# Kernel optimization log

Hardware: AMD Instinct MI355X
Metric: run time of the kernel (lower is better)

Reference implementation:

```python
import jax, jax.numpy as jnp
import numpy as np
from jax import lax

B, S, E, CC, H, NH, K = 8, 2048, 128, 256, 256, 8, 7
HD = H // NH  # head dim = 32


def setup_inputs() -> dict:
    key = jax.random.key(0)
    ks = jax.random.split(key, 16)
    x = jax.random.normal(ks[0], (B, S, E), dtype=jnp.float32)
    lengths = jax.random.randint(ks[1], (B,), S // 2, S + 1)
    mask = (jnp.arange(S)[None, :] < lengths[:, None])  # contiguous prefix padding mask
    sc = 0.02
    return {
        "x": x,
        "mask": mask,
        "conv_w": jax.random.normal(ks[2], (CC, E, K), dtype=jnp.float32) * sc,
        "conv_b": jnp.zeros((CC,), jnp.float32),
        "wq": jax.random.normal(ks[3], (CC, H), dtype=jnp.float32) * sc,
        "bq": jnp.zeros((H,), jnp.float32),
        "wk": jax.random.normal(ks[4], (CC, H), dtype=jnp.float32) * sc,
        "bk": jnp.zeros((H,), jnp.float32),
        "wv": jax.random.normal(ks[5], (CC, H), dtype=jnp.float32) * sc,
        "bv": jnp.zeros((H,), jnp.float32),
        "fc_w": jax.random.normal(ks[6], (H, CC), dtype=jnp.float32) * sc,
        "fc_b": jnp.zeros((CC,), jnp.float32),
        "ln_g": jnp.ones((CC,), jnp.float32),
        "ln_b": jnp.zeros((CC,), jnp.float32),
        "gamma": jnp.float32(0.5),
        "std_param": jnp.float32(0.2),
    }


def _penalty(mask, gamma, std_param):
    # (B, S, S) Gaussian penalty, nonzero only in the valid_len x valid_len block
    valid_len = mask.sum(axis=-1).astype(jnp.float32)  # (B,)
    idx = jnp.arange(S, dtype=jnp.float32)
    valid = (jnp.arange(S)[None, :] < mask.sum(axis=-1)[:, None]).astype(jnp.float32)  # (B,S)
    norm_pos = (idx[None, :] + 1.0) / (valid_len[:, None] + 1.0)  # (B,S)
    std = jnp.clip(std_param, 0.01, 0.5)
    base = jnp.exp(-((norm_pos - 0.5) ** 2) / (2.0 * std * std))
    pvec = base * (jnp.exp(gamma) - 1.0) * valid  # (B,S)
    pen = 0.5 * (pvec[:, :, None] + pvec[:, None, :])
    return pen * valid[:, :, None] * valid[:, None, :]


def reference(x, mask, conv_w, conv_b, wq, bq, wk, bk, wv, bv, fc_w, fc_b, ln_g, ln_b, gamma, std_param):
    # Conv1d frontend: (B,S,E) -> (B,E,S) -> conv -> relu -> (B,S,CC)
    xt = jnp.transpose(x, (0, 2, 1))
    y = lax.conv_general_dilated(xt, conv_w, window_strides=(1,), padding=[(K // 2, K // 2)])
    y = jax.nn.relu(y + conv_b[None, :, None])
    h = jnp.transpose(y, (0, 2, 1))  # (B,S,CC)

    q = (h @ wq + bq).reshape(B, S, NH, HD).transpose(0, 2, 1, 3)
    k = (h @ wk + bk).reshape(B, S, NH, HD).transpose(0, 2, 1, 3)
    v = (h @ wv + bv).reshape(B, S, NH, HD).transpose(0, 2, 1, 3)

    scores = jnp.einsum('bnqd,bnkd->bnqk', q, k) / np.sqrt(HD).astype(np.float32)
    scores = scores - _penalty(mask, gamma, std_param)[:, None, :, :]
    scores = jnp.where(mask[:, None, None, :], scores, jnp.float32(-1e10))
    probs = jax.nn.softmax(scores, axis=-1)
    ctx = jnp.einsum('bnqk,bnkd->bnqd', probs, v)
    ctx = ctx.transpose(0, 2, 1, 3).reshape(B, S, H)
    out = ctx @ fc_w + fc_b

    z = h + out
    mu = z.mean(-1, keepdims=True)
    var = ((z - mu) ** 2).mean(-1, keepdims=True)
    return (z - mu) / jnp.sqrt(var + 1e-5) * ln_g + ln_b
```

## Files before the change

kernel.cpp:

```cpp
#include <hip/hip_runtime.h>
#include <hip/hip_bf16.h>

#define B_ 8
#define S_ 2048
#define E_ 128
#define CC_ 256
#define H_ 256
#define NH_ 8
#define HD_ 32
#define KW_ 7

typedef __attribute__((ext_vector_type(8))) short bf16x8;
typedef __attribute__((ext_vector_type(4))) float f32x4;
typedef __attribute__((ext_vector_type(16))) float f32x16;

#define QSCALE_ (0.17677669529663687f * 1.4426950408889634f)
#define CPEN_   0.7213475204444817f

static __device__ __forceinline__ unsigned short f2bf(float f) {
    __hip_bfloat16 h = __float2bfloat16(f);
    return *(unsigned short*)&h;
}
static __device__ __forceinline__ float bf2f(unsigned short u) {
    __hip_bfloat16 h = *(__hip_bfloat16*)&u;
    return __bfloat162float(h);
}
static __device__ __forceinline__ void perm32swap(unsigned& a, unsigned& b) {
    asm volatile("s_nop 1\n\tv_permlane32_swap_b32 %0, %1" : "+v"(a), "+v"(b));
}

__global__ __launch_bounds__(256) void reorder_convw(
    const float* __restrict__ cw, unsigned short* __restrict__ wre2)
{
    int i = blockIdx.x * 256 + threadIdx.x;
    int kl = i & 31, cc = (i >> 5) & 255, eb = (i >> 13) & 3, kk = i >> 15;
    wre2[i] = f2bf(cw[cc * (E_ * KW_) + (eb * 32 + kl) * KW_ + kk]);
}
__global__ __launch_bounds__(256) void reorder_qkvw(
    const float* __restrict__ wq, const float* __restrict__ wk,
    const float* __restrict__ wv, unsigned short* __restrict__ wqkv2)
{
    int i = blockIdx.x * 256 + threadIdx.x;
    int kl = i & 31, col = (i >> 5) & 255, kb = (i >> 13) & 7, m = i >> 16;
    const float* W = (m == 0) ? wq : (m == 1) ? wk : wv;
    wqkv2[i] = f2bf(W[(kb * 32 + kl) * H_ + col]);
}
__global__ __launch_bounds__(256) void reorder_fcw(
    const float* __restrict__ fw, unsigned short* __restrict__ wf2)
{
    int i = blockIdx.x * 256 + threadIdx.x;
    int kl = i & 31, col = (i >> 5) & 255, kb = i >> 13;
    wf2[i] = f2bf(fw[(kb * 32 + kl) * CC_ + col]);
}

__global__ __launch_bounds__(256) void penalty_kernel(
    const void* __restrict__ mask, const float* __restrict__ gamma_p,
    const float* __restrict__ std_p, float* __restrict__ pvec,
    int* __restrict__ lenv)
{
    __shared__ int cnt[256];
    int b = blockIdx.x, tid = threadIdx.x;

    uint32_t w0 = ((const uint32_t*)mask)[0];
    int mode = 0;
    if (w0 == 0x01010101u) mode = 1;
    else if (w0 == 0x3F803F80u) mode = 2;
    else if (w0 == 0x3F800000u) mode = 3;

    int c = 0;
    for (int s = tid; s < S_; s += 256) {
        bool vv;
        size_t i = (size_t)b * S_ + s;
        if (mode == 0)      vv = ((const int*)mask)[i] != 0;
        else if (mode == 1) vv = ((const unsigned char*)mask)[i] != 0;
        else if (mode == 2) vv = (((const unsigned short*)mask)[i] & 0x7FFFu) != 0;
        else                vv = ((const float*)mask)[i] != 0.f;
        c += vv ? 1 : 0;
    }
    cnt[tid] = c;
    __syncthreads();
    for (int off = 128; off > 0; off >>= 1) {
        if (tid < off) cnt[tid] += cnt[tid + off];
        __syncthreads();
    }
    int L = cnt[0];
    if (tid == 0) lenv[b] = L;

    float Lf = (float)L;
    float gamma = gamma_p[0];
    float sd = std_p[0];
    sd = fminf(fmaxf(sd, 0.01f), 0.5f);
    float scale = expf(gamma) - 1.f;
    float inv2s2 = 1.f / (2.f * sd * sd);
    for (int s = tid; s < S_; s += 256) {
        float np = (s + 1.f) / (Lf + 1.f);
        float e = np - 0.5f;
        float base = expf(-(e * e) * inv2s2);
        pvec[(size_t)b * S_ + s] = (s < L) ? base * scale : 0.f;
    }
}

__global__ __launch_bounds__(256) void conv_mfma_kernel(
    const float* __restrict__ x, const unsigned short* __restrict__ wre2,
    const float* __restrict__ cb, unsigned short* __restrict__ hb)
{
    __shared__ short xl[70][136];
    const int tid = threadIdx.x, wave = tid >> 6, lane = tid & 63;
    const int l15 = lane & 15, l4 = lane >> 4;
    const int s0 = blockIdx.x * 64, b = blockIdx.y;

    for (int idx = tid; idx < 70 * 32; idx += 256) {
        int row = idx >> 5, c4 = idx & 31;
        int pos = s0 - 3 + row;
        float4 v = {0.f, 0.f, 0.f, 0.f};
        if (pos >= 0 && pos < S_)
            v = *(const float4*)(x + ((size_t)b * S_ + pos) * E_ + c4 * 4);
        short* p = &xl[row][c4 * 4];
        p[0] = (short)f2bf(v.x); p[1] = (short)f2bf(v.y);
        p[2] = (short)f2bf(v.z); p[3] = (short)f2bf(v.w);
    }
    __syncthreads();

    f32x4 acc[4][4];
#pragma unroll
    for (int i = 0; i < 4; i++)
#pragma unroll
        for (int j = 0; j < 4; j++) acc[i][j] = (f32x4){0.f, 0.f, 0.f, 0.f};

#pragma unroll 1
    for (int kk = 0; kk < KW_; kk++) {
#pragma unroll
        for (int eb = 0; eb < 4; eb++) {
            const unsigned short* wp =
                wre2 + (((size_t)(kk * 4 + eb) * 256 + wave * 64 + l15) * 32) + l4 * 8;
            bf16x8 af[4], bfr[4];
#pragma unroll
            for (int ct = 0; ct < 4; ct++)
                bfr[ct] = *(const bf16x8*)(wp + ct * 512);
#pragma unroll
            for (int rt = 0; rt < 4; rt++)
                af[rt] = *(const bf16x8*)(&xl[rt * 16 + l15 + kk][eb * 32 + l4 * 8]);
#pragma unroll
            for (int rt = 0; rt < 4; rt++)
#pragma unroll
                for (int ct = 0; ct < 4; ct++)
                    acc[rt][ct] = __builtin_amdgcn_mfma_f32_16x16x32_bf16(
                        af[rt], bfr[ct], acc[rt][ct], 0, 0, 0);
        }
    }

#pragma unroll
    for (int ct = 0; ct < 4; ct++) {
        int col = wave * 64 + ct * 16 + l15;
        float bias = cb[col];
#pragma unroll
        for (int rt = 0; rt < 4; rt++)
#pragma unroll
            for (int r = 0; r < 4; r++) {
                float v0 = acc[rt][ct][r] + bias;
                v0 = v0 > 0.f ? v0 : 0.f;
                int row = s0 + rt * 16 + l4 * 4 + r;
                hb[((size_t)b * S_ + row) * CC_ + col] = f2bf(v0);
            }
    }
}

__global__ __launch_bounds__(256) void qkv_mfma_kernel(
    const unsigned short* __restrict__ hb, const unsigned short* __restrict__ wqkv2,
    const float* __restrict__ bq, const float* __restrict__ bk,
    const float* __restrict__ bv,
    unsigned short* __restrict__ qo, unsigned short* __restrict__ ko,
    unsigned short* __restrict__ vo)
{
    __shared__ short Al[64][264];
    const int tid = threadIdx.x, wave = tid >> 6, lane = tid & 63;
    const int l15 = lane & 15, l4 = lane >> 4;
    const int s0 = blockIdx.x * 64, b = blockIdx.y;

    for (int idx = tid; idx < 64 * 32; idx += 256) {
        int row = idx >> 5, c8 = idx & 31;
        *(bf16x8*)(&Al[row][c8 * 8]) =
            *(const bf16x8*)(hb + ((size_t)b * S_ + s0 + row) * CC_ + c8 * 8);
    }
    __syncthreads();

#pragma unroll 1
    for (int m = 0; m < 3; m++) {
        f32x4 acc[4][4];
#pragma unroll
        for (int i = 0; i < 4; i++)
#pragma unroll
            for (int j = 0; j < 4; j++) acc[i][j] = (f32x4){0.f, 0.f, 0.f, 0.f};

#pragma unroll 1
        for (int kb8 = 0; kb8 < 8; kb8++) {
            const unsigned short* wp =
                wqkv2 + (((size_t)(m * 8 + kb8) * 256 + wave * 64 + l15) * 32) + l4 * 8;
            bf16x8 af[4], bfr[4];
#pragma unroll
            for (int ct = 0; ct < 4; ct++)
                bfr[ct] = *(const bf16x8*)(wp + ct * 512);
#pragma unroll
            for (int rt = 0; rt < 4; rt++)
                af[rt] = *(const bf16x8*)(&Al[rt * 16 + l15][kb8 * 32 + l4 * 8]);
#pragma unroll
            for (int rt = 0; rt < 4; rt++)
#pragma unroll
                for (int ct = 0; ct < 4; ct++)
                    acc[rt][ct] = __builtin_amdgcn_mfma_f32_16x16x32_bf16(
                        af[rt], bfr[ct], acc[rt][ct], 0, 0, 0);
        }

        const float* bias_p = (m == 0) ? bq : (m == 1) ? bk : bv;
        unsigned short* O = (m == 0) ? qo : (m == 1) ? ko : vo;
        const float oscale = (m == 0) ? QSCALE_ : 1.f;
#pragma unroll
        for (int ct = 0; ct < 4; ct++) {
            int col = wave * 64 + ct * 16 + l15;
            float bias = bias_p[col];
            int n = col >> 5, d = col & 31;
#pragma unroll
            for (int rt = 0; rt < 4; rt++)
#pragma unroll
                for (int r = 0; r < 4; r++) {
                    int row = s0 + rt * 16 + l4 * 4 + r;
                    O[(((size_t)b * NH_ + n) * S_ + row) * HD_ + d] =
                        f2bf((acc[rt][ct][r] + bias) * oscale);
                }
        }
    }
}

__global__ __launch_bounds__(256) void attn_mfma_kernel(
    const unsigned short* __restrict__ q, const unsigned short* __restrict__ k,
    const unsigned short* __restrict__ v, const float* __restrict__ pvec,
    const int* __restrict__ lenv, unsigned short* __restrict__ ctxb)
{
    __shared__ short Kt[2][128][40];
    __shared__ short Vt[2][32][136];
    __shared__ __align__(16) float ctC[2][2][128];

    const int tid = threadIdx.x;
    const int wave = tid >> 6, lane = tid & 63;
    const int r31 = lane & 31, hi = lane >> 5;
    const int hi8 = hi * 8, hi4 = hi * 4;
    const int n = blockIdx.y, b = blockIdx.z;
    const int qrow = blockIdx.x * 128 + wave * 32 + r31;
    const int L = lenv[b];
    const int nt = (L + 127) >> 7;

    const size_t head = ((size_t)b * NH_ + n) * S_;
    const unsigned short* qbase = q + head * HD_;
    const unsigned short* kbase = k + head * HD_;
    const unsigned short* vbase = v + head * HD_;

    bf16x8 qf0 = *(const bf16x8*)(qbase + (size_t)qrow * HD_ + hi8);
    bf16x8 qf1 = *(const bf16x8*)(qbase + (size_t)qrow * HD_ + 16 + hi8);
    const int crow = (qrow < L) ? 1 : 0;

    f32x16 acc;
#pragma unroll
    for (int r = 0; r < 16; r++) acc[r] = 0.f;
    float m_r = -1e30f, l_r = 0.f;

    const int krow = tid >> 1, kch = (tid & 1) * 16;
    const int d7x2 = 2 * (r31 & 7);
    const int vc = krow >> 3, vk7 = krow & 7;

    bf16x8 kreg0, kreg1, va, vb;
    float pvr = 0.f;

    kreg0 = *(const bf16x8*)(kbase + (size_t)krow * HD_ + kch);
    kreg1 = *(const bf16x8*)(kbase + (size_t)krow * HD_ + kch + 8);
    va    = *(const bf16x8*)(vbase + (size_t)krow * HD_ + kch);
    vb    = *(const bf16x8*)(vbase + (size_t)krow * HD_ + kch + 8);
    if (tid < 128) pvr = pvec[(size_t)b * S_ + tid];
    {
        *(bf16x8*)(&Kt[0][krow][kch])     = kreg0;
        *(bf16x8*)(&Kt[0][krow][kch + 8]) = kreg1;
#pragma unroll
        for (int i = 0; i < 8; i++) {
            int d0 = kch + i, d1 = kch + 8 + i;
            Vt[0][d0][((((vc - 2 * (d0 & 7)) & 7) | (vc & 8)) << 3) + vk7] = va[i];
            Vt[0][d1][((((vc - 2 * (d1 & 7)) & 7) | (vc & 8)) << 3) + vk7] = vb[i];
        }
        if (tid < 128) {
            bool vkk = tid < L;
            ctC[0][0][tid] = vkk ? 0.f : -1e10f;
            ctC[0][1][tid] = vkk ? (-CPEN_ * pvr) : -1e10f;
        }
    }
    __syncthreads();

#pragma unroll 1
    for (int t = 0; t < nt; t++) {
        const int cur = t & 1;
        const int knext = (t + 1) << 7;
        const bool more = (t + 1 < nt);

        if (more) {
            kreg0 = *(const bf16x8*)(kbase + (size_t)(knext + krow) * HD_ + kch);
            kreg1 = *(const bf16x8*)(kbase + (size_t)(knext + krow) * HD_ + kch + 8);
            va    = *(const bf16x8*)(vbase + (size_t)(knext + krow) * HD_ + kch);
            vb    = *(const bf16x8*)(vbase + (size_t)(knext + krow) * HD_ + kch + 8);
            if (tid < 128) pvr = pvec[(size_t)b * S_ + knext + tid];
        }

        __builtin_amdgcn_s_setprio(1);
        f32x16 sc[4];
#pragma unroll
        for (int t4 = 0; t4 < 4; t4++) {
            bf16x8 kf0 = *(const bf16x8*)(&Kt[cur][t4 * 32 + r31][hi8]);
            bf16x8 kf1 = *(const bf16x8*)(&Kt[cur][t4 * 32 + r31][16 + hi8]);
            f32x16 c0;
#pragma unroll
            for (int g = 0; g < 4; g++) {
                f32x4 cp = *(const f32x4*)(&ctC[cur][crow][t4 * 32 + g * 8 + hi4]);
#pragma unroll
                for (int j = 0; j < 4; j++) c0[g * 4 + j] = cp[j];
            }
            f32x16 s1 = __builtin_amdgcn_mfma_f32_32x32x16_bf16(kf0, qf0, c0, 0, 0, 0);
            sc[t4] = __builtin_amdgcn_mfma_f32_32x32x16_bf16(kf1, qf1, s1, 0, 0, 0);
        }
        __builtin_amdgcn_s_setprio(0);

        float pmx = -1e30f;
#pragma unroll
        for (int t4 = 0; t4 < 4; t4++)
#pragma unroll
            for (int r = 0; r < 16; r += 2)
                pmx = fmaxf(pmx, fmaxf(sc[t4][r], sc[t4][r + 1]));
        pmx = fmaxf(pmx, __shfl_xor(pmx, 32, 64));

        float alpha = 1.f;
        if (!__all(pmx <= m_r + 8.f)) {
            float mn = fmaxf(m_r, pmx);
            alpha = exp2f(m_r - mn);
            m_r = mn;
#pragma unroll
            for (int r = 0; r < 16; r++) acc[r] *= alpha;
        }

        float rs = 0.f;
        unsigned pk[4][8];
#pragma unroll
        for (int t4 = 0; t4 < 4; t4++) {
            float p[16];
#pragma unroll
            for (int r = 0; r < 16; r++) {
                p[r] = exp2f(sc[t4][r] - m_r);
                rs += p[r];
            }
            unsigned U00 = (unsigned)f2bf(p[0])  | ((unsigned)f2bf(p[1])  << 16);
            unsigned U01 = (unsigned)f2bf(p[2])  | ((unsigned)f2bf(p[3])  << 16);
            unsigned U10 = (unsigned)f2bf(p[4])  | ((unsigned)f2bf(p[5])  << 16);
            unsigned U11 = (unsigned)f2bf(p[6])  | ((unsigned)f2bf(p[7])  << 16);
            unsigned U20 = (unsigned)f2bf(p[8])  | ((unsigned)f2bf(p[9])  << 16);
            unsigned U21 = (unsigned)f2bf(p[10]) | ((unsigned)f2bf(p[11]) << 16);
            unsigned U30 = (unsigned)f2bf(p[12]) | ((unsigned)f2bf(p[13]) << 16);
            unsigned U31 = (unsigned)f2bf(p[14]) | ((unsigned)f2bf(p[15]) << 16);
            perm32swap(U00, U10);
            perm32swap(U01, U11);
            perm32swap(U20, U30);
            perm32swap(U21, U31);
            pk[t4][0] = U00; pk[t4][1] = U01; pk[t4][2] = U10; pk[t4][3] = U11;
            pk[t4][4] = U20; pk[t4][5] = U21; pk[t4][6] = U30; pk[t4][7] = U31;
        }
        rs += __shfl_xor(rs, 32, 64);
        l_r = l_r * alpha + rs;

        __builtin_amdgcn_s_setprio(1);
#pragma unroll
        for (int t4 = 0; t4 < 4; t4++) {
            union { unsigned u[4]; bf16x8 v8; } pb0, pb1;
            pb0.u[0] = pk[t4][0]; pb0.u[1] = pk[t4][1];
            pb0.u[2] = pk[t4][2]; pb0.u[3] = pk[t4][3];
            pb1.u[0] = pk[t4][4]; pb1.u[1] = pk[t4][5];
            pb1.u[2] = pk[t4][6]; pb1.u[3] = pk[t4][7];
            int c0i = t4 * 4 + hi, c1i = t4 * 4 + 2 + hi;
            bf16x8 vf0 = *(const bf16x8*)(&Vt[cur][r31][(((c0i - d7x2) & 7) | (c0i & 8)) << 3]);
            bf16x8 vf1 = *(const bf16x8*)(&Vt[cur][r31][(((c1i - d7x2) & 7) | (c1i & 8)) << 3]);
            acc = __builtin_amdgcn_mfma_f32_32x32x16_bf16(vf0, pb0.v8, acc, 0, 0, 0);
            acc = __builtin_amdgcn_mfma_f32_32x32x16_bf16(vf1, pb1.v8, acc, 0, 0, 0);
        }
        __builtin_amdgcn_s_setprio(0);

        if (more) {
            const int nxt = cur ^ 1;
            *(bf16x8*)(&Kt[nxt][krow][kch])     = kreg0;
            *(bf16x8*)(&Kt[nxt][krow][kch + 8]) = kreg1;
#pragma unroll
            for (int i = 0; i < 8; i++) {
                int d0 = kch + i, d1 = kch + 8 + i;
                Vt[nxt][d0][((((vc - 2 * (d0 & 7)) & 7) | (vc & 8)) << 3) + vk7] = va[i];
                Vt[nxt][d1][((((vc - 2 * (d1 & 7)) & 7) | (vc & 8)) << 3) + vk7] = vb[i];
            }
            if (tid < 128) {
                bool vkk = (knext + tid) < L;
                ctC[nxt][0][tid] = vkk ? 0.f : -1e10f;
                ctC[nxt][1][tid] = vkk ? (-CPEN_ * pvr) : -1e10f;
            }
            __syncthreads();
        }
    }

    float inv = 1.f / l_r;
    size_t obase = ((size_t)b * S_ + qrow) * H_ + n * HD_;
#pragma unroll
    for (int g = 0; g < 4; g++)
#pragma unroll
        for (int w = 0; w < 2; w++) {
            unsigned uo = (unsigned)f2bf(acc[g * 4 + w * 2] * inv) |
                          ((unsigned)f2bf(acc[g * 4 + w * 2 + 1] * inv) << 16);
            int d = 8 * g + hi4 + 2 * w;
            *(unsigned*)(ctxb + obase + d) = uo;
        }
}

__global__ __launch_bounds__(256) void fc_ln_mfma_kernel(
    const unsigned short* __restrict__ ctxb, const unsigned short* __restrict__ hb,
    const unsigned short* __restrict__ wf2, const float* __restrict__ fb,
    const float* __restrict__ g, const float* __restrict__ bbias,
    float* __restrict__ out)
{
    const int tid = threadIdx.x, wave = tid >> 6, lane = tid & 63;
    const int l15 = lane & 15, l4 = lane >> 4;
    const int s0 = blockIdx.x * 64, b = blockIdx.y;
    const int arow = s0 + wave * 16 + l15;

    bf16x8 af[8];
#pragma unroll
    for (int kb = 0; kb < 8; kb++)
        af[kb] = *(const bf16x8*)(ctxb + (size_t)((size_t)b * S_ + arow) * H_ + kb * 32 + l4 * 8);

    f32x4 acc[16];
#pragma unroll
    for (int ct = 0; ct < 16; ct++) acc[ct] = (f32x4){0.f, 0.f, 0.f, 0.f};

#pragma unroll 1
    for (int kb = 0; kb < 8; kb++) {
        const unsigned short* wp = wf2 + ((size_t)kb * 256 + l15) * 32 + l4 * 8;
#pragma unroll
        for (int ct = 0; ct < 16; ct++) {
            bf16x8 bfr = *(const bf16x8*)(wp + ct * 512);
            acc[ct] = __builtin_amdgcn_mfma_f32_16x16x32_bf16(af[kb], bfr, acc[ct], 0, 0, 0);
        }
    }

    float fbias[16];
#pragma unroll
    for (int ct = 0; ct < 16; ct++) fbias[ct] = fb[ct * 16 + l15];

#pragma unroll
    for (int r = 0; r < 4; r++) {
        int row = s0 + wave * 16 + l4 * 4 + r;
        size_t ro = ((size_t)b * S_ + row) * CC_;
        float z[16];
        float sum = 0.f;
#pragma unroll
        for (int ct = 0; ct < 16; ct++) {
            float zz = acc[ct][r] + fbias[ct] + bf2f(hb[ro + ct * 16 + l15]);
            z[ct] = zz;
            sum += zz;
        }
#pragma unroll
        for (int off = 1; off < 16; off <<= 1) sum += __shfl_xor(sum, off, 64);
        float mu = sum * (1.f / 256.f);
        float vs = 0.f;
#pragma unroll
        for (int ct = 0; ct < 16; ct++) {
            float d = z[ct] - mu;
            z[ct] = d;
            vs += d * d;
        }
#pragma unroll
        for (int off = 1; off < 16; off <<= 1) vs += __shfl_xor(vs, off, 64);
        float inv = rsqrtf(vs * (1.f / 256.f) + 1e-5f);
#pragma unroll
        for (int ct = 0; ct < 16; ct++) {
            int col = ct * 16 + l15;
            out[ro + col] = z[ct] * inv * g[col] + bbias[col];
        }
    }
}

extern "C" void kernel_launch(void* const* d_in, const int* in_sizes, int n_in,
                              void* d_out, int out_size, void* d_ws, size_t ws_size,
                              hipStream_t stream)
{
    const float* x      = (const float*)d_in[0];
    const void*  mask   = d_in[1];
    const float* conv_w = (const float*)d_in[2];
    const float* conv_b = (const float*)d_in[3];
    const float* wq     = (const float*)d_in[4];
    const float* bq     = (const float*)d_in[5];
    const float* wk     = (const float*)d_in[6];
    const float* bk     = (const float*)d_in[7];
    const float* wv     = (const float*)d_in[8];
    const float* bv     = (const float*)d_in[9];
    const float* fc_w   = (const float*)d_in[10];
    const float* fc_b   = (const float*)d_in[11];
    const float* ln_g   = (const float*)d_in[12];
    const float* ln_b   = (const float*)d_in[13];
    const float* gamma  = (const float*)d_in[14];
    const float* stdp   = (const float*)d_in[15];

    char* ws = (char*)d_ws;
    const size_t MB = 1024 * 1024;
    unsigned short* hb    = (unsigned short*)(ws);
    unsigned short* qb    = (unsigned short*)(ws + 8 * MB);
    unsigned short* kb    = (unsigned short*)(ws + 16 * MB);
    unsigned short* vb    = (unsigned short*)(ws + 24 * MB);
    unsigned short* ctxb  = (unsigned short*)(ws + 32 * MB);
    float*          pvec  = (float*)(ws + 40 * MB);
    int*            lenv  = (int*)(ws + 40 * MB + 64 * 1024);
    unsigned short* wre2  = (unsigned short*)(ws + 41 * MB);
    unsigned short* wqkv2 = (unsigned short*)(ws + 42 * MB);
    unsigned short* wf2   = (unsigned short*)(ws + 43 * MB);

    reorder_convw<<<896, 256, 0, stream>>>(conv_w, wre2);
    reorder_qkvw<<<768, 256, 0, stream>>>(wq, wk, wv, wqkv2);
    reorder_fcw<<<256, 256, 0, stream>>>(fc_w, wf2);
    penalty_kernel<<<B_, 256, 0, stream>>>(mask, gamma, stdp, pvec, lenv);

    dim3 g2(S_ / 64, B_);
    conv_mfma_kernel<<<g2, 256, 0, stream>>>(x, wre2, conv_b, hb);
    qkv_mfma_kernel<<<g2, 256, 0, stream>>>(hb, wqkv2, bq, bk, bv, qb, kb, vb);
    dim3 ag(S_ / 128, NH_, B_);
    attn_mfma_kernel<<<ag, 256, 0, stream>>>(qb, kb, vb, pvec, lenv, ctxb);
    fc_ln_mfma_kernel<<<g2, 256, 0, stream>>>(ctxb, hb, wf2, fc_b, ln_g, ln_b,
                                              (float*)d_out);
}
```

Before: 200.6 us.

## Merge prep kernels, fuse conv with QKV, precompute mask/penalty table, remap attention grid

```diff
diff --git a/kernel.cpp b/kernel.cpp
--- a/kernel.cpp
+++ b/kernel.cpp
@@ -11,6 +11,7 @@
 #define KW_ 7
 
 typedef __attribute__((ext_vector_type(8))) short bf16x8;
+typedef __attribute__((ext_vector_type(2))) float f32x2;
 typedef __attribute__((ext_vector_type(4))) float f32x4;
 typedef __attribute__((ext_vector_type(16))) float f32x16;
 
@@ -29,82 +30,90 @@
     asm volatile("s_nop 1\n\tv_permlane32_swap_b32 %0, %1" : "+v"(a), "+v"(b));
 }
 
-__global__ __launch_bounds__(256) void reorder_convw(
-    const float* __restrict__ cw, unsigned short* __restrict__ wre2)
-{
-    int i = blockIdx.x * 256 + threadIdx.x;
-    int kl = i & 31, cc = (i >> 5) & 255, eb = (i >> 13) & 3, kk = i >> 15;
-    wre2[i] = f2bf(cw[cc * (E_ * KW_) + (eb * 32 + kl) * KW_ + kk]);
-}
-__global__ __launch_bounds__(256) void reorder_qkvw(
-    const float* __restrict__ wq, const float* __restrict__ wk,
-    const float* __restrict__ wv, unsigned short* __restrict__ wqkv2)
-{
-    int i = blockIdx.x * 256 + threadIdx.x;
-    int kl = i & 31, col = (i >> 5) & 255, kb = (i >> 13) & 7, m = i >> 16;
-    const float* W = (m == 0) ? wq : (m == 1) ? wk : wv;
-    wqkv2[i] = f2bf(W[(kb * 32 + kl) * H_ + col]);
-}
-__global__ __launch_bounds__(256) void reorder_fcw(
-    const float* __restrict__ fw, unsigned short* __restrict__ wf2)
-{
-    int i = blockIdx.x * 256 + threadIdx.x;
-    int kl = i & 31, col = (i >> 5) & 255, kb = i >> 13;
-    wf2[i] = f2bf(fw[(kb * 32 + kl) * CC_ + col]);
-}
-
-__global__ __launch_bounds__(256) void penalty_kernel(
-    const void* __restrict__ mask, const float* __restrict__ gamma_p,
-    const float* __restrict__ std_p, float* __restrict__ pvec,
+__global__ __launch_bounds__(256) void prep_kernel(
+    const float* __restrict__ cw, const float* __restrict__ wq,
+    const float* __restrict__ wk, const float* __restrict__ wv,
+    const float* __restrict__ fw, const void* __restrict__ mask,
+    const float* __restrict__ gamma_p, const float* __restrict__ std_p,
+    unsigned short* __restrict__ wre2, unsigned short* __restrict__ wqkv2,
+    unsigned short* __restrict__ wf2, float* __restrict__ ctab,
     int* __restrict__ lenv)
 {
     __shared__ int cnt[256];
-    int b = blockIdx.x, tid = threadIdx.x;
-
-    uint32_t w0 = ((const uint32_t*)mask)[0];
-    int mode = 0;
-    if (w0 == 0x01010101u) mode = 1;
-    else if (w0 == 0x3F803F80u) mode = 2;
-    else if (w0 == 0x3F800000u) mode = 3;
-
-    int c = 0;
-    for (int s = tid; s < S_; s += 256) {
-        bool vv;
-        size_t i = (size_t)b * S_ + s;
-        if (mode == 0)      vv = ((const int*)mask)[i] != 0;
-        else if (mode == 1) vv = ((const unsigned char*)mask)[i] != 0;
-        else if (mode == 2) vv = (((const unsigned short*)mask)[i] & 0x7FFFu) != 0;
-        else                vv = ((const float*)mask)[i] != 0.f;
-        c += vv ? 1 : 0;
-    }
-    cnt[tid] = c;
-    __syncthreads();
-    for (int off = 128; off > 0; off >>= 1) {
-        if (tid < off) cnt[tid] += cnt[tid + off];
+    const int blk = blockIdx.x, tid = threadIdx.x;
+
+    if (blk < 896) {
+        int i = blk * 256 + tid;
+        int kl = i & 31, cc = (i >> 5) & 255, eb = (i >> 13) & 3, kk = i >> 15;
+        wre2[i] = f2bf(cw[cc * (E_ * KW_) + (eb * 32 + kl) * KW_ + kk]);
+    } else if (blk < 1664) {
+        int i = (blk - 896) * 256 + tid;
+        int kl = i & 31, col = (i >> 5) & 255, kb = (i >> 13) & 7, m = i >> 16;
+        const float* W = (m == 0) ? wq : (m == 1) ? wk : wv;
+        wqkv2[i] = f2bf(W[(kb * 32 + kl) * H_ + col]);
+    } else if (blk < 1920) {
+        int i = (blk - 1664) * 256 + tid;
+        int kl = i & 31, col = (i >> 5) & 255, kb = i >> 13;
+        wf2[i] = f2bf(fw[(kb * 32 + kl) * CC_ + col]);
+    } else {
+        int b = blk - 1920;
+
+        uint32_t w0 = ((const uint32_t*)mask)[0];
+        int mode = 0;
+        if (w0 == 0x01010101u) mode = 1;
+        else if (w0 == 0x3F803F80u) mode = 2;
+        else if (w0 == 0x3F800000u) mode = 3;
+
+        int c = 0;
+        for (int s = tid; s < S_; s += 256) {
+            bool vv;
+            size_t i = (size_t)b * S_ + s;
+            if (mode == 0)      vv = ((const int*)mask)[i] != 0;
+            else if (mode == 1) vv = ((const unsigned char*)mask)[i] != 0;
+            else if (mode == 2) vv = (((const unsigned short*)mask)[i] & 0x7FFFu) != 0;
+            else                vv = ((const float*)mask)[i] != 0.f;
+            c += vv ? 1 : 0;
+        }
+        cnt[tid] = c;
         __syncthreads();
-    }
-    int L = cnt[0];
-    if (tid == 0) lenv[b] = L;
-
-    float Lf = (float)L;
-    float gamma = gamma_p[0];
-    float sd = std_p[0];
-    sd = fminf(fmaxf(sd, 0.01f), 0.5f);
-    float scale = expf(gamma) - 1.f;
-    float inv2s2 = 1.f / (2.f * sd * sd);
-    for (int s = tid; s < S_; s += 256) {
-        float np = (s + 1.f) / (Lf + 1.f);
-        float e = np - 0.5f;
-        float base = expf(-(e * e) * inv2s2);
-        pvec[(size_t)b * S_ + s] = (s < L) ? base * scale : 0.f;
-    }
-}
-
-__global__ __launch_bounds__(256) void conv_mfma_kernel(
+        for (int off = 128; off > 0; off >>= 1) {
+            if (tid < off) cnt[tid] += cnt[tid + off];
+            __syncthreads();
+        }
+        int L = cnt[0];
+        if (tid == 0) lenv[b] = L;
+
+        float Lf = (float)L;
+        float gamma = gamma_p[0];
+        float sd = std_p[0];
+        sd = fminf(fmaxf(sd, 0.01f), 0.5f);
+        float scale = expf(gamma) - 1.f;
+        float inv2s2 = 1.f / (2.f * sd * sd);
+        float* row0 = ctab + (size_t)b * 2 * S_;
+        float* row1 = row0 + S_;
+        for (int s = tid; s < S_; s += 256) {
+            float np = (s + 1.f) / (Lf + 1.f);
+            float e = np - 0.5f;
+            float base = expf(-(e * e) * inv2s2);
+            bool vkk = s < L;
+            row0[s] = vkk ? 0.f : -1e10f;
+            row1[s] = vkk ? (-CPEN_ * base * scale) : -1e10f;
+        }
+    }
+}
+
+__global__ __launch_bounds__(256) void front_kernel(
     const float* __restrict__ x, const unsigned short* __restrict__ wre2,
-    const float* __restrict__ cb, unsigned short* __restrict__ hb)
+    const float* __restrict__ cb, const unsigned short* __restrict__ wqkv2,
+    const float* __restrict__ bq, const float* __restrict__ bk,
+    const float* __restrict__ bv, unsigned short* __restrict__ hb,
+    unsigned short* __restrict__ qo, unsigned short* __restrict__ ko,
+    unsigned short* __restrict__ vo)
 {
-    __shared__ short xl[70][136];
+    __shared__ __align__(16) char smem[64 * 264 * 2];
+    short (*xl)[136] = (short(*)[136])smem;
+    short (*Al)[264] = (short(*)[264])smem;
+
     const int tid = threadIdx.x, wave = tid >> 6, lane = tid & 63;
     const int l15 = lane & 15, l4 = lane >> 4;
     const int s0 = blockIdx.x * 64, b = blockIdx.y;
@@ -148,6 +157,7 @@
                         af[rt], bfr[ct], acc[rt][ct], 0, 0, 0);
         }
     }
+    __syncthreads();
 
 #pragma unroll
     for (int ct = 0; ct < 4; ct++) {
@@ -159,38 +169,24 @@
             for (int r = 0; r < 4; r++) {
                 float v0 = acc[rt][ct][r] + bias;
                 v0 = v0 > 0.f ? v0 : 0.f;
-                int row = s0 + rt * 16 + l4 * 4 + r;
-                hb[((size_t)b * S_ + row) * CC_ + col] = f2bf(v0);
+                Al[rt * 16 + l4 * 4 + r][col] = (short)f2bf(v0);
             }
     }
-}
-
-__global__ __launch_bounds__(256) void qkv_mfma_kernel(
-    const unsigned short* __restrict__ hb, const unsigned short* __restrict__ wqkv2,
-    const float* __restrict__ bq, const float* __restrict__ bk,
-    const float* __restrict__ bv,
-    unsigned short* __restrict__ qo, unsigned short* __restrict__ ko,
-    unsigned short* __restrict__ vo)
-{
-    __shared__ short Al[64][264];
-    const int tid = threadIdx.x, wave = tid >> 6, lane = tid & 63;
-    const int l15 = lane & 15, l4 = lane >> 4;
-    const int s0 = blockIdx.x * 64, b = blockIdx.y;
+    __syncthreads();
 
     for (int idx = tid; idx < 64 * 32; idx += 256) {
         int row = idx >> 5, c8 = idx & 31;
-        *(bf16x8*)(&Al[row][c8 * 8]) =
-            *(const bf16x8*)(hb + ((size_t)b * S_ + s0 + row) * CC_ + c8 * 8);
-    }
-    __syncthreads();
+        *(bf16x8*)(hb + ((size_t)b * S_ + s0 + row) * CC_ + c8 * 8) =
+            *(const bf16x8*)(&Al[row][c8 * 8]);
+    }
 
 #pragma unroll 1
     for (int m = 0; m < 3; m++) {
-        f32x4 acc[4][4];
+        f32x4 qacc[4][4];
 #pragma unroll
         for (int i = 0; i < 4; i++)
 #pragma unroll
-            for (int j = 0; j < 4; j++) acc[i][j] = (f32x4){0.f, 0.f, 0.f, 0.f};
+            for (int j = 0; j < 4; j++) qacc[i][j] = (f32x4){0.f, 0.f, 0.f, 0.f};
 
 #pragma unroll 1
         for (int kb8 = 0; kb8 < 8; kb8++) {
@@ -207,8 +203,8 @@
             for (int rt = 0; rt < 4; rt++)
 #pragma unroll
                 for (int ct = 0; ct < 4; ct++)
-                    acc[rt][ct] = __builtin_amdgcn_mfma_f32_16x16x32_bf16(
-                        af[rt], bfr[ct], acc[rt][ct], 0, 0, 0);
+                    qacc[rt][ct] = __builtin_amdgcn_mfma_f32_16x16x32_bf16(
+                        af[rt], bfr[ct], qacc[rt][ct], 0, 0, 0);
         }
 
         const float* bias_p = (m == 0) ? bq : (m == 1) ? bk : bv;
@@ -225,7 +221,7 @@
                 for (int r = 0; r < 4; r++) {
                     int row = s0 + rt * 16 + l4 * 4 + r;
                     O[(((size_t)b * NH_ + n) * S_ + row) * HD_ + d] =
-                        f2bf((acc[rt][ct][r] + bias) * oscale);
+                        f2bf((qacc[rt][ct][r] + bias) * oscale);
                 }
         }
     }
@@ -233,19 +229,20 @@
 
 __global__ __launch_bounds__(256) void attn_mfma_kernel(
     const unsigned short* __restrict__ q, const unsigned short* __restrict__ k,
-    const unsigned short* __restrict__ v, const float* __restrict__ pvec,
+    const unsigned short* __restrict__ v, const float* __restrict__ ctab,
     const int* __restrict__ lenv, unsigned short* __restrict__ ctxb)
 {
     __shared__ short Kt[2][128][40];
     __shared__ short Vt[2][32][136];
-    __shared__ __align__(16) float ctC[2][2][128];
 
     const int tid = threadIdx.x;
     const int wave = tid >> 6, lane = tid & 63;
     const int r31 = lane & 31, hi = lane >> 5;
     const int hi8 = hi * 8, hi4 = hi * 4;
-    const int n = blockIdx.y, b = blockIdx.z;
-    const int qrow = blockIdx.x * 128 + wave * 32 + r31;
+
+    const int idx = blockIdx.x;
+    const int b = (idx >> 3) & 7, n = idx & 7, qt = idx >> 6;
+    const int qrow = qt * 128 + wave * 32 + r31;
     const int L = lenv[b];
     const int nt = (L + 127) >> 7;
 
@@ -256,7 +253,7 @@
 
     bf16x8 qf0 = *(const bf16x8*)(qbase + (size_t)qrow * HD_ + hi8);
     bf16x8 qf1 = *(const bf16x8*)(qbase + (size_t)qrow * HD_ + 16 + hi8);
-    const int crow = (qrow < L) ? 1 : 0;
+    const float* ct_row = ctab + ((size_t)b * 2 + ((qrow < L) ? 1 : 0)) * S_;
 
     f32x16 acc;
 #pragma unroll
@@ -268,13 +265,11 @@
     const int vc = krow >> 3, vk7 = krow & 7;
 
     bf16x8 kreg0, kreg1, va, vb;
-    float pvr = 0.f;
 
     kreg0 = *(const bf16x8*)(kbase + (size_t)krow * HD_ + kch);
     kreg1 = *(const bf16x8*)(kbase + (size_t)krow * HD_ + kch + 8);
     va    = *(const bf16x8*)(vbase + (size_t)krow * HD_ + kch);
     vb    = *(const bf16x8*)(vbase + (size_t)krow * HD_ + kch + 8);
-    if (tid < 128) pvr = pvec[(size_t)b * S_ + tid];
     {
         *(bf16x8*)(&Kt[0][krow][kch])     = kreg0;
         *(bf16x8*)(&Kt[0][krow][kch + 8]) = kreg1;
@@ -283,11 +278,6 @@
             int d0 = kch + i, d1 = kch + 8 + i;
             Vt[0][d0][((((vc - 2 * (d0 & 7)) & 7) | (vc & 8)) << 3) + vk7] = va[i];
             Vt[0][d1][((((vc - 2 * (d1 & 7)) & 7) | (vc & 8)) << 3) + vk7] = vb[i];
-        }
-        if (tid < 128) {
-            bool vkk = tid < L;
-            ctC[0][0][tid] = vkk ? 0.f : -1e10f;
-            ctC[0][1][tid] = vkk ? (-CPEN_ * pvr) : -1e10f;
         }
     }
     __syncthreads();
@@ -303,7 +293,6 @@
             kreg1 = *(const bf16x8*)(kbase + (size_t)(knext + krow) * HD_ + kch + 8);
             va    = *(const bf16x8*)(vbase + (size_t)(knext + krow) * HD_ + kch);
             vb    = *(const bf16x8*)(vbase + (size_t)(knext + krow) * HD_ + kch + 8);
-            if (tid < 128) pvr = pvec[(size_t)b * S_ + knext + tid];
         }
 
         __builtin_amdgcn_s_setprio(1);
@@ -315,7 +304,7 @@
             f32x16 c0;
 #pragma unroll
             for (int g = 0; g < 4; g++) {
-                f32x4 cp = *(const f32x4*)(&ctC[cur][crow][t4 * 32 + g * 8 + hi4]);
+                f32x4 cp = *(const f32x4*)(ct_row + ((t << 7) + t4 * 32 + g * 8 + hi4));
 #pragma unroll
                 for (int j = 0; j < 4; j++) c0[g * 4 + j] = cp[j];
             }
@@ -341,31 +330,28 @@
             for (int r = 0; r < 16; r++) acc[r] *= alpha;
         }
 
-        float rs = 0.f;
+        f32x2 rs2 = {0.f, 0.f};
+        const f32x2 m2 = {m_r, m_r};
         unsigned pk[4][8];
 #pragma unroll
         for (int t4 = 0; t4 < 4; t4++) {
-            float p[16];
-#pragma unroll
-            for (int r = 0; r < 16; r++) {
-                p[r] = exp2f(sc[t4][r] - m_r);
-                rs += p[r];
+            unsigned U[8];
+#pragma unroll
+            for (int j = 0; j < 8; j++) {
+                f32x2 s2 = { sc[t4][2 * j], sc[t4][2 * j + 1] };
+                s2 = s2 - m2;
+                f32x2 p2 = { exp2f(s2.x), exp2f(s2.y) };
+                rs2 += p2;
+                U[j] = (unsigned)f2bf(p2.x) | ((unsigned)f2bf(p2.y) << 16);
             }
-            unsigned U00 = (unsigned)f2bf(p[0])  | ((unsigned)f2bf(p[1])  << 16);
-            unsigned U01 = (unsigned)f2bf(p[2])  | ((unsigned)f2bf(p[3])  << 16);
-            unsigned U10 = (unsigned)f2bf(p[4])  | ((unsigned)f2bf(p[5])  << 16);
-            unsigned U11 = (unsigned)f2bf(p[6])  | ((unsigned)f2bf(p[7])  << 16);
-            unsigned U20 = (unsigned)f2bf(p[8])  | ((unsigned)f2bf(p[9])  << 16);
-            unsigned U21 = (unsigned)f2bf(p[10]) | ((unsigned)f2bf(p[11]) << 16);
-            unsigned U30 = (unsigned)f2bf(p[12]) | ((unsigned)f2bf(p[13]) << 16);
-            unsigned U31 = (unsigned)f2bf(p[14]) | ((unsigned)f2bf(p[15]) << 16);
-            perm32swap(U00, U10);
-            perm32swap(U01, U11);
-            perm32swap(U20, U30);
-            perm32swap(U21, U31);
-            pk[t4][0] = U00; pk[t4][1] = U01; pk[t4][2] = U10; pk[t4][3] = U11;
-            pk[t4][4] = U20; pk[t4][5] = U21; pk[t4][6] = U30; pk[t4][7] = U31;
-        }
+            perm32swap(U[0], U[2]);
+            perm32swap(U[1], U[3]);
+            perm32swap(U[4], U[6]);
+            perm32swap(U[5], U[7]);
+            pk[t4][0] = U[0]; pk[t4][1] = U[1]; pk[t4][2] = U[2]; pk[t4][3] = U[3];
+            pk[t4][4] = U[4]; pk[t4][5] = U[5]; pk[t4][6] = U[6]; pk[t4][7] = U[7];
+        }
+        float rs = rs2.x + rs2.y;
         rs += __shfl_xor(rs, 32, 64);
         l_r = l_r * alpha + rs;
 
@@ -394,11 +380,6 @@
                 int d0 = kch + i, d1 = kch + 8 + i;
                 Vt[nxt][d0][((((vc - 2 * (d0 & 7)) & 7) | (vc & 8)) << 3) + vk7] = va[i];
                 Vt[nxt][d1][((((vc - 2 * (d1 & 7)) & 7) | (vc & 8)) << 3) + vk7] = vb[i];
-            }
-            if (tid < 128) {
-                bool vkk = (knext + tid) < L;
-                ctC[nxt][0][tid] = vkk ? 0.f : -1e10f;
-                ctC[nxt][1][tid] = vkk ? (-CPEN_ * pvr) : -1e10f;
             }
             __syncthreads();
         }
@@ -512,22 +493,19 @@
     unsigned short* kb    = (unsigned short*)(ws + 16 * MB);
     unsigned short* vb    = (unsigned short*)(ws + 24 * MB);
     unsigned short* ctxb  = (unsigned short*)(ws + 32 * MB);
-    float*          pvec  = (float*)(ws + 40 * MB);
-    int*            lenv  = (int*)(ws + 40 * MB + 64 * 1024);
+    float*          ctab  = (float*)(ws + 40 * MB);
+    int*            lenv  = (int*)(ws + 40 * MB + 256 * 1024);
     unsigned short* wre2  = (unsigned short*)(ws + 41 * MB);
     unsigned short* wqkv2 = (unsigned short*)(ws + 42 * MB);
     unsigned short* wf2   = (unsigned short*)(ws + 43 * MB);
 
-    reorder_convw<<<896, 256, 0, stream>>>(conv_w, wre2);
-    reorder_qkvw<<<768, 256, 0, stream>>>(wq, wk, wv, wqkv2);
-    reorder_fcw<<<256, 256, 0, stream>>>(fc_w, wf2);
-    penalty_kernel<<<B_, 256, 0, stream>>>(mask, gamma, stdp, pvec, lenv);
-
+    prep_kernel<<<1928, 256, 0, stream>>>(conv_w, wq, wk, wv, fc_w, mask,
+                                          gamma, stdp, wre2, wqkv2, wf2,
+                                          ctab, lenv);
     dim3 g2(S_ / 64, B_);
-    conv_mfma_kernel<<<g2, 256, 0, stream>>>(x, wre2, conv_b, hb);
-    qkv_mfma_kernel<<<g2, 256, 0, stream>>>(hb, wqkv2, bq, bk, bv, qb, kb, vb);
-    dim3 ag(S_ / 128, NH_, B_);
-    attn_mfma_kernel<<<ag, 256, 0, stream>>>(qb, kb, vb, pvec, lenv, ctxb);
+    front_kernel<<<g2, 256, 0, stream>>>(x, wre2, conv_b, wqkv2, bq, bk, bv,
+                                         hb, qb, kb, vb);
+    attn_mfma_kernel<<<1024, 256, 0, stream>>>(qb, kb, vb, ctab, lenv, ctxb);
     fc_ln_mfma_kernel<<<g2, 256, 0, stream>>>(ctxb, hb, wf2, fc_b, ln_g, ln_b,
                                               (float*)d_out);
 }
```

Measured after the change: 237.9 us. +18.6%, slower.
